# Optimization experiments

Measured on AMD Instinct MI355X. Metric: run time of the kernel, lower is better.

The kernel has to match this reference:

```python
import jax, jax.numpy as jnp
import numpy as np

DIM = 32
B, H, W = 4, 256, 256


def conv1x1(x, w, b):
    # x: [B,C,H,W], w: [O,C], b: [O]
    return jnp.einsum('bchw,oc->bohw', x, w) + b[None, :, None, None]


def conv3x3(x, w, b):
    # x: [B,C,H,W], w: [O,C,3,3]
    out = jax.lax.conv_general_dilated(
        x, w, window_strides=(1, 1), padding='SAME',
        dimension_numbers=('NCHW', 'OIHW', 'NCHW'))
    return out + b[None, :, None, None]


def fft2d(x):
    # fft2 over last two dims, then fftshift over ALL dims (torch default)
    f = jnp.fft.fftshift(jnp.fft.fft2(x, norm='ortho'))
    return jnp.concatenate([f.real, f.imag], axis=1)  # [B,2C,H,W]


def ifft2d(x):
    f = jnp.fft.ifftshift(x)  # over ALL dims (torch default)
    re, im = jnp.split(f, 2, axis=1)
    c = jax.lax.complex(re, im)
    return jnp.abs(jnp.fft.ifft2(c, norm='ortho'))  # [B,C,H,W]


def setup_inputs() -> dict:
    key = jax.random.key(0)
    ks = jax.random.split(key, 16)
    C = DIM
    s = 0.02  # small init keeps the global-HW dot products in a sane softmax range
    inp = {
        'x': jax.random.normal(ks[0], (B, C, H, W), jnp.float32),
        'y': jax.random.normal(ks[1], (B, C, H, W), jnp.float32),
        'wq': jax.random.normal(ks[2], (C, C), jnp.float32) * s,
        'bq': jnp.zeros((C,), jnp.float32),
        'wk': jax.random.normal(ks[3], (C, C), jnp.float32) * s,
        'bk': jnp.zeros((C,), jnp.float32),
        'wv': jax.random.normal(ks[4], (C, C), jnp.float32) * s,
        'bv': jnp.zeros((C,), jnp.float32),
        'wd': jax.random.normal(ks[5], (C, C), jnp.float32) * s,
        'bd': jnp.zeros((C,), jnp.float32),
        'wc': jax.random.normal(ks[6], (2 * C, 2 * C, 3, 3), jnp.float32) * s,
        'bc': jnp.zeros((2 * C,), jnp.float32),
        'wi': jax.random.normal(ks[7], (2 * C, 2 * C, 3, 3), jnp.float32) * s,
        'bi': jnp.zeros((2 * C,), jnp.float32),
    }
    return inp


def reference(x, y, wq, bq, wk, bk, wv, bv, wd, bd, wc, bc, wi, bi):
    b, c, h, w = x.shape
    xq = conv1x1(x, wq, bq).reshape(b, c, h * w)            # [B,C,HW]
    dft = conv3x3(fft2d(conv1x1(y, wd, bd)), wc, bc)        # [B,2C,H,W]
    yk, yv = jnp.split(dft, 2, axis=1)
    yk = conv1x1(yk, wk, bk).reshape(b, c, h * w)
    yv = conv1x1(yv, wv, bv).reshape(b, c, h * w)
    att = jnp.einsum('bcn,bdn->bcd', xq, yk)                # [B,C,C]
    att = jax.nn.softmax(att, axis=1)                       # softmax over dim=1 (as in torch)
    out = jnp.einsum('bcd,bdn->bcn', att, yv).reshape(b, c, h, w)
    out = out + ifft2d(conv3x3(jax.nn.relu(dft), wi, bi))
    return out
```

## Files before the change

### kernel.cpp

```cpp
#include <hip/hip_runtime.h>
#include <math.h>

#define HW_ (256*256)
#define CH 32
#define CH2 64
#define BATCH 4

typedef short bf16x8 __attribute__((ext_vector_type(8)));
typedef float f32x4 __attribute__((ext_vector_type(4)));

__device__ __forceinline__ unsigned short f2bf(float f) {
    union { float f; unsigned u; } v; v.f = f;
    unsigned r = v.u + 0x7fffu + ((v.u >> 16) & 1u);
    return (unsigned short)(r >> 16);
}
__device__ __forceinline__ float bf2f(unsigned h) {
    union { unsigned u; float f; } v; v.u = h << 16;
    return v.f;
}

__device__ __forceinline__ int ctof_slot(int s) {
    return s < 16 ? s + 16 : s < 32 ? s + 32 : s < 48 ? s - 32 : s - 16;
}

__device__ __forceinline__ float2 cmul(float2 a, float2 b) {
    return make_float2(a.x*b.x - a.y*b.y, a.x*b.y + a.y*b.x);
}

__device__ __forceinline__ void build_tw4(float2* tw, float sign) {
    int tid = threadIdx.x;
    float ang = sign * 6.2831853071795864769f * (float)tid / 256.0f;
    float s, c; sincosf(ang, &s, &c);
    tw[tid] = make_float2(c, s);
}

template<int SGN>
__device__ __forceinline__ void fft16_reg(float2* x, const float2* tw) {
    float2 u[16];
    #pragma unroll
    for (int m0 = 0; m0 < 4; ++m0) {
        float2 x0 = x[m0], x1 = x[m0+4], x2 = x[m0+8], x3 = x[m0+12];
        float2 t0 = make_float2(x0.x+x2.x, x0.y+x2.y);
        float2 t1 = make_float2(x0.x-x2.x, x0.y-x2.y);
        float2 t2 = make_float2(x1.x+x3.x, x1.y+x3.y);
        float2 t3 = make_float2(x1.x-x3.x, x1.y-x3.y);
        float2 r  = make_float2(-SGN*t3.y, SGN*t3.x);
        u[m0*4+0] = make_float2(t0.x+t2.x, t0.y+t2.y);
        u[m0*4+1] = make_float2(t1.x+r.x,  t1.y+r.y);
        u[m0*4+2] = make_float2(t0.x-t2.x, t0.y-t2.y);
        u[m0*4+3] = make_float2(t1.x-r.x,  t1.y-r.y);
    }
    #pragma unroll
    for (int m0 = 1; m0 < 4; ++m0)
        #pragma unroll
        for (int a = 1; a < 4; ++a)
            u[m0*4+a] = cmul(u[m0*4+a], tw[(16*m0*a) & 255]);
    #pragma unroll
    for (int a = 0; a < 4; ++a) {
        float2 x0 = u[a], x1 = u[4+a], x2 = u[8+a], x3 = u[12+a];
        float2 t0 = make_float2(x0.x+x2.x, x0.y+x2.y);
        float2 t1 = make_float2(x0.x-x2.x, x0.y-x2.y);
        float2 t2 = make_float2(x1.x+x3.x, x1.y+x3.y);
        float2 t3 = make_float2(x1.x-x3.x, x1.y-x3.y);
        float2 r  = make_float2(-SGN*t3.y, SGN*t3.x);
        x[a]    = make_float2(t0.x+t2.x, t0.y+t2.y);
        x[a+4]  = make_float2(t1.x+r.x,  t1.y+r.y);
        x[a+8]  = make_float2(t0.x-t2.x, t0.y-t2.y);
        x[a+12] = make_float2(t1.x-r.x,  t1.y-r.y);
    }
}

template<int SGN>
__device__ __forceinline__ void fft_core16(float2* A, const float2* tw) {
    const int tid = threadIdx.x;
    const int l = tid >> 4;
    const int d = tid & 15;
    const int base = l*257;
    float2 x[16];
    #pragma unroll
    for (int n1 = 0; n1 < 16; ++n1) x[n1] = A[base + n1*16 + d];
    fft16_reg<SGN>(x, tw);
    #pragma unroll
    for (int k0 = 1; k0 < 16; ++k0) x[k0] = cmul(x[k0], tw[d*k0]);
    #pragma unroll
    for (int k0 = 0; k0 < 16; ++k0) A[base + k0*16 + ((d + k0) & 15)] = x[k0];
    __syncthreads();
    #pragma unroll
    for (int n0 = 0; n0 < 16; ++n0) x[n0] = A[base + d*16 + ((n0 + d) & 15)];
    fft16_reg<SGN>(x, tw);
    #pragma unroll
    for (int k1 = 0; k1 < 16; ++k1) A[base + d + k1*16] = x[k1];
    __syncthreads();
}

__global__ __launch_bounds__(256) void k_fft_fwd1(const unsigned short* __restrict__ yd, ushort2* __restrict__ CAt) {
    __shared__ float2 A[16*257];
    __shared__ float2 tw[256];
    build_tw4(tw, -1.0f);
    int blk = blockIdx.x;
    int bc = blk >> 4, h0 = (blk & 15) << 4;
    const float sc = 1.0f/16.0f;
    const unsigned short* src = yd + (size_t)bc*HW_ + (size_t)h0*256;
    for (int idx = threadIdx.x; idx < 16*256; idx += 256) {
        int l = idx >> 8, w = idx & 255;
        A[l*257 + w] = make_float2(bf2f(src[l*256 + w])*sc, 0.0f);
    }
    __syncthreads();
    fft_core16<-1>(A, tw);
    int t = threadIdx.x;
    ushort2* dst = CAt + (size_t)bc*HW_ + (size_t)t*256 + h0;
    #pragma unroll
    for (int l = 0; l < 16; ++l) {
        float2 v = A[l*257 + t];
        dst[l] = make_ushort2(f2bf(v.x), f2bf(v.y));
    }
}

__global__ __launch_bounds__(256) void k_fft_fwd2(const ushort2* __restrict__ CAt, unsigned short* __restrict__ FSH) {
    __shared__ float2 A[16*257];
    __shared__ float2 tw[256];
    build_tw4(tw, -1.0f);
    int blk = blockIdx.x;
    int b = blk >> 9, chalf = (blk >> 8) & 1, w = blk & 255;
    const float sc = 1.0f/16.0f;
    const ushort2* src = CAt + (((size_t)(b*32 + chalf*16))*256 + w)*256;
    for (int idx = threadIdx.x; idx < 16*256; idx += 256) {
        int l = idx >> 8, h = idx & 255;
        ushort2 v = src[(size_t)l*HW_ + h];
        A[l*257 + h] = make_float2(bf2f(v.x)*sc, bf2f(v.y)*sc);
    }
    __syncthreads();
    fft_core16<-1>(A, tw);
    int t = threadIdx.x;
    int bt = (b + 2) & 3;
    int ht = (t + 128) & 255;
    int wt = (w + 128) & 255;
    unsigned short pk[32];
    #pragma unroll
    for (int l = 0; l < 16; ++l) {
        float2 v = A[l*257 + t];
        pk[l]      = f2bf(v.x);
        pk[16 + l] = f2bf(v.y);
    }
    unsigned short* dst = FSH + ((((size_t)bt*256 + ht)*256 + wt)*64 + chalf*32);
    uint4* d4 = (uint4*)dst;
    const uint4* s4 = (const uint4*)pk;
    d4[0] = s4[0]; d4[1] = s4[1]; d4[2] = s4[2]; d4[3] = s4[3];
}

__global__ __launch_bounds__(256) void k_wpack2(const float* __restrict__ wc, const float* __restrict__ wi,
                                                unsigned short* __restrict__ d1, unsigned short* __restrict__ d2) {
    int i = blockIdx.x*256 + threadIdx.x;
    int half = i >= 36864;
    int j = i - half*36864;
    int tap = j >> 12, rem = j & 4095, oc = rem >> 6, s = rem & 63;
    if (half) {
        d2[j] = f2bf(wi[((size_t)(oc*64 + s))*9 + tap]);
    } else {
        int ic = ctof_slot(s);
        d1[j] = f2bf(wc[((size_t)(oc*64 + ic))*9 + tap]);
    }
}

template<int MODE>
__global__ __launch_bounds__(256) void k_conv3(const unsigned short* __restrict__ in_cl,
                                               const unsigned short* __restrict__ wpk,
                                               const float* __restrict__ bias,
                                               unsigned short* __restrict__ outp) {
    __shared__ __align__(16) char Xs[3168*16];
    int tid = threadIdx.x;
    int blk = blockIdx.x;
    int wseg = blk & 3, hg = (blk >> 2) & 63, b = blk >> 8;
    int h0 = hg*4, w0 = wseg*64;

    for (int gl = tid; gl < 3168; gl += 256) {
        int slot = gl / 528;
        int rem  = gl - slot*528;
        int col  = rem >> 3, hseg = rem & 7;
        int hh = h0 - 1 + slot;
        int wcol = w0 - 1 + col;
        uint4 v = make_uint4(0,0,0,0);
        if (hh >= 0 && hh < 256 && wcol >= 0 && wcol < 256) {
            v = *(const uint4*)(in_cl + (((size_t)(b*256 + hh)*256 + wcol)*64) + hseg*8);
            if (MODE == 1) {
                unsigned* pv = (unsigned*)&v;
                #pragma unroll
                for (int q = 0; q < 4; ++q) {
                    unsigned a = pv[q];
                    unsigned lo = a & 0xffffu, hi = a >> 16;
                    if (lo & 0x8000u) lo = 0;
                    if (hi & 0x8000u) hi = 0;
                    pv[q] = lo | (hi << 16);
                }
            }
        }
        *(uint4*)(Xs + ((gl << 4) ^ ((col & 7) << 4))) = v;
    }
    __syncthreads();

    int lane = tid & 63;
    int wv = tid >> 6;
    int l16 = lane & 15, lq = lane >> 4;

    f32x4 acc[4][4];
    #pragma unroll
    for (int i = 0; i < 4; ++i)
        #pragma unroll
        for (int j = 0; j < 4; ++j) acc[i][j] = (f32x4)0.0f;

    #pragma unroll
    for (int dy = 0; dy < 3; ++dy) {
        int slot = wv + dy;
        #pragma unroll
        for (int dx = 0; dx < 3; ++dx) {
            int tap = dy*3 + dx;
            #pragma unroll
            for (int kk = 0; kk < 2; ++kk) {
                int hseg = kk*4 + lq;
                bf16x8 xf[4], wf[4];
                #pragma unroll
                for (int j = 0; j < 4; ++j) {
                    int col = j*16 + l16 + dx;
                    int g = slot*528 + col*8 + hseg;
                    xf[j] = *(const bf16x8*)(Xs + ((g << 4) ^ ((col & 7) << 4)));
                }
                #pragma unroll
                for (int i = 0; i < 4; ++i) {
                    int oc = i*16 + l16;
                    wf[i] = *(const bf16x8*)(wpk + (size_t)tap*4096 + oc*64 + hseg*8);
                    #pragma unroll
                    for (int j = 0; j < 4; ++j) {
                        if (MODE == 0)
                            acc[i][j] = __builtin_amdgcn_mfma_f32_16x16x32_bf16(wf[i], xf[j], acc[i][j], 0, 0, 0);
                        else
                            acc[i][j] = __builtin_amdgcn_mfma_f32_16x16x32_bf16(xf[j], wf[i], acc[i][j], 0, 0, 0);
                    }
                }
            }
        }
    }

    int h = h0 + wv;
    if (MODE == 0) {
        #pragma unroll
        for (int j = 0; j < 4; ++j) {
            int px = w0 + j*16 + l16;
            unsigned short* orow = outp + (((size_t)b*256 + h)*256 + px)*64;
            #pragma unroll
            for (int i = 0; i < 4; ++i) {
                int oc0 = i*16 + lq*4;
                float4 bv = *(const float4*)(bias + oc0);
                unsigned short c0 = f2bf(acc[i][j][0] + bv.x);
                unsigned short c1 = f2bf(acc[i][j][1] + bv.y);
                unsigned short c2 = f2bf(acc[i][j][2] + bv.z);
                unsigned short c3 = f2bf(acc[i][j][3] + bv.w);
                uint2 u;
                u.x = (unsigned)c0 | ((unsigned)c1 << 16);
                u.y = (unsigned)c2 | ((unsigned)c3 << 16);
                *(uint2*)(orow + oc0) = u;
            }
        }
    } else {
        #pragma unroll
        for (int i = 0; i < 4; ++i) {
            int oc = i*16 + l16;
            float bv = bias[oc];
            unsigned short* oplane = outp + ((size_t)b*64 + oc)*HW_ + (size_t)h*256;
            #pragma unroll
            for (int j = 0; j < 4; ++j) {
                int px0 = w0 + j*16 + lq*4;
                unsigned short c0 = f2bf(acc[i][j][0] + bv);
                unsigned short c1 = f2bf(acc[i][j][1] + bv);
                unsigned short c2 = f2bf(acc[i][j][2] + bv);
                unsigned short c3 = f2bf(acc[i][j][3] + bv);
                uint2 u;
                u.x = (unsigned)c0 | ((unsigned)c1 << 16);
                u.y = (unsigned)c2 | ((unsigned)c3 << 16);
                *(uint2*)(oplane + px0) = u;
            }
        }
    }
}

__global__ __launch_bounds__(256) void k_conv1x1(const float* __restrict__ in, const float* __restrict__ w,
                                                 const float* __restrict__ bias, unsigned short* __restrict__ out) {
    __shared__ float ts[32*257];
    int blk = blockIdx.x; int b = blk >> 8, h = blk & 255;
    int tid = threadIdx.x;
    const float* src = in + (size_t)b*CH*HW_ + (size_t)h*256;
    for (int idx = tid; idx < 32*256; idx += 256) {
        int c = idx >> 8, ww = idx & 255;
        ts[c*257 + ww] = src[(size_t)c*HW_ + ww];
    }
    __syncthreads();
    float acc[32];
    #pragma unroll
    for (int o = 0; o < 32; ++o) acc[o] = bias[o];
    for (int c = 0; c < 32; ++c) {
        float v = ts[c*257 + tid];
        #pragma unroll
        for (int o = 0; o < 32; ++o) acc[o] += w[o*32 + c] * v;
    }
    unsigned short* dst = out + (size_t)b*CH*HW_ + (size_t)h*256 + tid;
    #pragma unroll
    for (int o = 0; o < 32; ++o) dst[(size_t)o*HW_] = f2bf(acc[o]);
}

__global__ __launch_bounds__(256) void k_gram(const float* __restrict__ x, const unsigned short* __restrict__ dcl,
                                              float* __restrict__ Mpart, float* __restrict__ Sxp, float* __restrict__ Sdp) {
    __shared__ float mred[1024];
    __shared__ float sxred[32];
    __shared__ float sdred[32];
    int blk = blockIdx.x;
    int b = blk >> 7, chunk = blk & 127;
    int tid = threadIdx.x, lane = tid & 63, wv = tid >> 6;
    int l16 = lane & 15, lq = lane >> 4;
    for (int idx = tid; idx < 1024; idx += 256) mred[idx] = 0.0f;
    if (tid < 32) { sxred[tid] = 0.0f; sdred[tid] = 0.0f; }
    __syncthreads();

    const float* xb0 = x + (size_t)b*CH*HW_ + (size_t)l16*HW_;
    const float* xb1 = xb0 + (size_t)16*HW_;
    const unsigned short* db = dcl + (size_t)b*HW_*64;

    f32x4 acc[2][2];
    #pragma unroll
    for (int i = 0; i < 2; ++i)
        #pragma unroll
        for (int j = 0; j < 2; ++j) acc[i][j] = (f32x4)0.0f;
    float sx0 = 0, sx1 = 0, sd0 = 0, sd1 = 0;

    int pxw = chunk*512 + wv*128;
    #pragma unroll
    for (int ks = 0; ks < 4; ++ks) {
        int px = pxw + ks*32 + lq*8;
        float4 xa = *(const float4*)(xb0 + px);
        float4 xc = *(const float4*)(xb0 + px + 4);
        float4 ya = *(const float4*)(xb1 + px);
        float4 yc = *(const float4*)(xb1 + px + 4);
        bf16x8 a0, a1, b0, b1;
        const float* pxa = (const float*)&xa;
        const float* pxc = (const float*)&xc;
        const float* pya = (const float*)&ya;
        const float* pyc = (const float*)&yc;
        #pragma unroll
        for (int j = 0; j < 4; ++j) {
            a0[j]   = (short)f2bf(pxa[j]);  sx0 += pxa[j];
            a0[4+j] = (short)f2bf(pxc[j]);  sx0 += pxc[j];
            a1[j]   = (short)f2bf(pya[j]);  sx1 += pya[j];
            a1[4+j] = (short)f2bf(pyc[j]);  sx1 += pyc[j];
        }
        const unsigned short* dbp = db + (size_t)px*64 + l16;
        #pragma unroll
        for (int j = 0; j < 8; ++j) {
            unsigned short v0 = dbp[j*64];
            unsigned short v1 = dbp[j*64 + 16];
            b0[j] = (short)v0;  sd0 += bf2f(v0);
            b1[j] = (short)v1;  sd1 += bf2f(v1);
        }
        acc[0][0] = __builtin_amdgcn_mfma_f32_16x16x32_bf16(a0, b0, acc[0][0], 0, 0, 0);
        acc[0][1] = __builtin_amdgcn_mfma_f32_16x16x32_bf16(a0, b1, acc[0][1], 0, 0, 0);
        acc[1][0] = __builtin_amdgcn_mfma_f32_16x16x32_bf16(a1, b0, acc[1][0], 0, 0, 0);
        acc[1][1] = __builtin_amdgcn_mfma_f32_16x16x32_bf16(a1, b1, acc[1][1], 0, 0, 0);
    }

    #pragma unroll
    for (int fi = 0; fi < 2; ++fi)
        #pragma unroll
        for (int fj = 0; fj < 2; ++fj)
            #pragma unroll
            for (int r = 0; r < 4; ++r)
                atomicAdd(&mred[(fi*16 + lq*4 + r)*32 + fj*16 + l16], acc[fi][fj][r]);

    sx0 += __shfl_xor(sx0, 16); sx0 += __shfl_xor(sx0, 32);
    sx1 += __shfl_xor(sx1, 16); sx1 += __shfl_xor(sx1, 32);
    sd0 += __shfl_xor(sd0, 16); sd0 += __shfl_xor(sd0, 32);
    sd1 += __shfl_xor(sd1, 16); sd1 += __shfl_xor(sd1, 32);
    if (lane < 16) {
        atomicAdd(&sxred[l16], sx0);
        atomicAdd(&sxred[l16 + 16], sx1);
        atomicAdd(&sdred[l16], sd0);
        atomicAdd(&sdred[l16 + 16], sd1);
    }
    __syncthreads();

    float* mp = Mpart + ((size_t)(b*128 + chunk))*1024;
    for (int idx = tid; idx < 1024; idx += 256) mp[idx] = mred[idx];
    if (tid < 32) {
        Sxp[(b*128 + chunk)*32 + tid] = sxred[tid];
        Sdp[(b*128 + chunk)*32 + tid] = sdred[tid];
    }
}

__global__ __launch_bounds__(256) void k_att(const float* __restrict__ Mpart, const float* __restrict__ Sxp,
                                              const float* __restrict__ Sdp,
                                              const float* __restrict__ wq, const float* __restrict__ bq,
                                              const float* __restrict__ wk, const float* __restrict__ bk,
                                              const float* __restrict__ wv, const float* __restrict__ bv,
                                              float* __restrict__ att2, float* __restrict__ sout) {
    __shared__ float Mls[1024], T1[1024], attls[32*33];
    __shared__ float wqs[1024], wks[1024], wvs[1024];
    __shared__ float q1[32], k1[32], sxs[32], sds[32];
    int tid = threadIdx.x;
    int b = blockIdx.x;
    for (int idx = tid; idx < 1024; idx += 256) { wqs[idx] = wq[idx]; wks[idx] = wk[idx]; wvs[idx] = wv[idx]; }
    #pragma unroll
    for (int q = 0; q < 4; ++q) {
        int o = tid + q*256;
        float s = 0;
        for (int c = 0; c < 128; ++c) s += Mpart[((size_t)(b*128 + c))*1024 + o];
        Mls[o] = s;
    }
    if (tid < 32) { float s = 0; for (int c = 0; c < 128; ++c) s += Sxp[(b*128 + c)*32 + tid]; sxs[tid] = s; }
    else if (tid < 64) { int e = tid - 32; float s = 0; for (int c = 0; c < 128; ++c) s += Sdp[(b*128 + c)*32 + e]; sds[e] = s; }
    __syncthreads();
    if (tid < 32) { float s=0; for (int a=0;a<32;++a) s += wqs[tid*32+a]*sxs[a]; q1[tid]=s; }
    else if (tid < 64) { int d=tid-32; float s=0; for (int e=0;e<32;++e) s += wks[d*32+e]*sds[e]; k1[d]=s; }
    for (int idx = tid; idx < 1024; idx += 256) {
        int c = idx >> 5, e = idx & 31;
        float s = 0;
        for (int a=0;a<32;++a) s += wqs[c*32+a]*Mls[a*32+e];
        T1[idx] = s;
    }
    __syncthreads();
    for (int idx = tid; idx < 1024; idx += 256) {
        int c = idx >> 5, d = idx & 31;
        float s = 0;
        for (int e=0;e<32;++e) s += T1[c*32+e]*wks[d*32+e];
        s += bq[c]*k1[d] + bk[d]*q1[c] + 65536.0f*bq[c]*bk[d];
        attls[c*33+d] = s;
    }
    __syncthreads();
    if (tid < 32) {
        int d = tid;
        float mx = -1e30f;
        for (int c=0;c<32;++c) mx = fmaxf(mx, attls[c*33+d]);
        float sum = 0;
        for (int c=0;c<32;++c) { float e_ = expf(attls[c*33+d]-mx); attls[c*33+d]=e_; sum+=e_; }
        float inv = 1.0f/sum;
        for (int c=0;c<32;++c) attls[c*33+d] *= inv;
    }
    __syncthreads();
    for (int idx = tid; idx < 1024; idx += 256) {
        int c = idx >> 5, e = idx & 31;
        float s = 0;
        for (int d=0; d<32; ++d) s += attls[c*33+d]*wvs[d*32+e];
        att2[b*1024 + idx] = s;
    }
    if (tid < 32) {
        float s=0; for (int d=0;d<32;++d) s += attls[tid*33+d]*bv[d];
        sout[b*32+tid] = s;
    }
}

__global__ __launch_bounds__(256) void k_fft_inv1(const unsigned short* __restrict__ G, ushort2* __restrict__ Z1T) {
    __shared__ float2 A[16*257];
    __shared__ float2 tw[256];
    build_tw4(tw, 1.0f);
    int blk = blockIdx.x;
    int bc = blk >> 4, w0 = (blk & 15) << 4;
    int b = bc >> 5, c = bc & 31;
    int bs = (b + 2) & 3;
    const float sc = 1.0f/16.0f;
    const unsigned short* gre = G + ((size_t)(bs*CH2 + c + 32))*HW_;
    const unsigned short* gim = G + ((size_t)(bs*CH2 + c))*HW_;
    for (int idx = threadIdx.x; idx < 16*256; idx += 256) {
        int h = idx >> 4, l = idx & 15;
        int hs = (h + 128) & 255;
        int ws = (w0 + l + 128) & 255;
        A[l*257 + h] = make_float2(bf2f(gre[(size_t)hs*256 + ws])*sc, bf2f(gim[(size_t)hs*256 + ws])*sc);
    }
    __syncthreads();
    fft_core16<1>(A, tw);
    ushort2* dst = Z1T + (size_t)bc*HW_;
    for (int idx = threadIdx.x; idx < 16*256; idx += 256) {
        int l = idx >> 8, h = idx & 255;
        float2 v = A[l*257 + h];
        dst[(size_t)(w0 + l)*256 + h] = make_ushort2(f2bf(v.x), f2bf(v.y));
    }
}

__global__ __launch_bounds__(256) void k_fft_inv2(const ushort2* __restrict__ Z1T, unsigned short* __restrict__ Mag) {
    __shared__ float2 A[16*257];
    __shared__ float2 tw[256];
    build_tw4(tw, 1.0f);
    int blk = blockIdx.x;
    int bc = blk >> 4, h0 = (blk & 15) << 4;
    const float sc = 1.0f/16.0f;
    const ushort2* src = Z1T + (size_t)bc*HW_ + h0;
    for (int idx = threadIdx.x; idx < 16*256; idx += 256) {
        int w = idx >> 4, l = idx & 15;
        ushort2 v = src[(size_t)w*256 + l];
        A[l*257 + w] = make_float2(bf2f(v.x)*sc, bf2f(v.y)*sc);
    }
    __syncthreads();
    fft_core16<1>(A, tw);
    unsigned short* dst = Mag + (size_t)bc*HW_ + (size_t)h0*256;
    for (int idx = threadIdx.x; idx < 16*256; idx += 256) {
        int l = idx >> 8, w = idx & 255;
        float2 v = A[l*257 + w];
        dst[l*256 + w] = f2bf(sqrtf(v.x*v.x + v.y*v.y));
    }
}

__global__ __launch_bounds__(256) void k_out(const unsigned short* __restrict__ dcl, const float* __restrict__ att2,
                                             const float* __restrict__ sv, const unsigned short* __restrict__ Mag,
                                             float* __restrict__ out) {
    __shared__ __align__(16) float A2ls[1024];
    __shared__ float svls[32];
    int blk = blockIdx.x; int b = blk >> 8, h = blk & 255;
    int tid = threadIdx.x;
    for (int idx = tid; idx < 1024; idx += 256) A2ls[idx] = att2[b*1024 + idx];
    if (tid < 32) svls[tid] = sv[b*32 + tid];
    __syncthreads();
    int px = tid;
    const uint4* dvp = (const uint4*)(dcl + ((((size_t)b*256 + h)*256 + px)*64 + 32));
    uint4 d0 = dvp[0], d1 = dvp[1];
    unsigned u[8] = {d0.x, d0.y, d0.z, d0.w, d1.x, d1.y, d1.z, d1.w};
    float dv[32];
    #pragma unroll
    for (int i = 0; i < 8; ++i) {
        dv[2*i]   = bf2f(u[i] & 0xffffu);
        dv[2*i+1] = bf2f(u[i] >> 16);
    }
    float accv[32];
    #pragma unroll
    for (int c = 0; c < 32; ++c) accv[c] = svls[c];
    #pragma unroll
    for (int q = 0; q < 8; ++q) {
        #pragma unroll
        for (int c = 0; c < 32; ++c) {
            float4 a4 = *(const float4*)&A2ls[c*32 + q*4];
            accv[c] += a4.x*dv[q*4] + a4.y*dv[q*4+1] + a4.z*dv[q*4+2] + a4.w*dv[q*4+3];
        }
    }
    const unsigned short* mb = Mag + (size_t)b*CH*HW_ + (size_t)h*256 + px;
    float* ob = out + (size_t)b*CH*HW_ + (size_t)h*256 + px;
    #pragma unroll
    for (int c = 0; c < 32; ++c) ob[(size_t)c*HW_] = accv[c] + bf2f(mb[(size_t)c*HW_]);
}

extern "C" void kernel_launch(void* const* d_in, const int* in_sizes, int n_in,
                              void* d_out, int out_size, void* d_ws, size_t ws_size,
                              hipStream_t stream) {
    const float* x  = (const float*)d_in[0];
    const float* y  = (const float*)d_in[1];
    const float* wq = (const float*)d_in[2];
    const float* bq = (const float*)d_in[3];
    const float* wk = (const float*)d_in[4];
    const float* bk = (const float*)d_in[5];
    const float* wv = (const float*)d_in[6];
    const float* bv = (const float*)d_in[7];
    const float* wd = (const float*)d_in[8];
    const float* bd = (const float*)d_in[9];
    const float* wc = (const float*)d_in[10];
    const float* bc = (const float*)d_in[11];
    const float* wi = (const float*)d_in[12];
    const float* bi = (const float*)d_in[13];
    float* out = (float*)d_out;

    char* ws = (char*)d_ws;
    size_t o = 0;
    unsigned short* R1   = (unsigned short*)(ws + o); o += (size_t)BATCH*CH*HW_*2;
    ushort2*        CAt  = (ushort2*)(ws + o);        o += (size_t)BATCH*CH*HW_*4;
    unsigned short* FSHc = (unsigned short*)(ws + o); o += (size_t)BATCH*CH2*HW_*2;
    unsigned short* DFTc = (unsigned short*)(ws + o); o += (size_t)BATCH*CH2*HW_*2;
    unsigned short* Gpl  = (unsigned short*)(ws + o); o += (size_t)BATCH*CH2*HW_*2;
    unsigned short* wpk1 = (unsigned short*)(ws + o); o += 9*64*64*2;
    unsigned short* wpk2 = (unsigned short*)(ws + o); o += 9*64*64*2;
    float*          Mpart= (float*)(ws + o);          o += (size_t)512*1024*4;
    float*          Sxp  = (float*)(ws + o);          o += 512*32*4;
    float*          Sdp  = (float*)(ws + o);          o += 512*32*4;
    float*          A2b  = (float*)(ws + o);          o += 4096*4;
    float*          Svb  = (float*)(ws + o);          o += 128*4;
    if (ws_size < o) return;

    ushort2*        Z1T = CAt;
    unsigned short* Mag = R1;

    k_wpack2<<<288, 256, 0, stream>>>(wc, wi, wpk1, wpk2);
    k_conv1x1<<<1024, 256, 0, stream>>>(y, wd, bd, R1);
    k_fft_fwd1<<<2048, 256, 0, stream>>>(R1, CAt);
    k_fft_fwd2<<<2048, 256, 0, stream>>>(CAt, FSHc);
    k_conv3<0><<<1024, 256, 0, stream>>>(FSHc, wpk1, bc, DFTc);
    k_conv3<1><<<1024, 256, 0, stream>>>(DFTc, wpk2, bi, Gpl);
    k_gram<<<512, 256, 0, stream>>>(x, DFTc, Mpart, Sxp, Sdp);
    k_att<<<4, 256, 0, stream>>>(Mpart, Sxp, Sdp, wq, bq, wk, bk, wv, bv, A2b, Svb);
    k_fft_inv1<<<2048, 256, 0, stream>>>(Gpl, Z1T);
    k_fft_inv2<<<2048, 256, 0, stream>>>(Z1T, Mag);
    k_out<<<1024, 256, 0, stream>>>(DFTc, A2b, Svb, Mag, out);
}
```

Measured before the change: 319.5 us.

## Stage conv3x3 weights in LDS and prefetch input rows per dy step

The 3x3 conv kernel now keeps one dy-row of weights (3 taps) in shared memory and only 4 of the 6 input rows in a ring buffer. It register-prefetches the next input row and weight slice from global memory while the MFMAs for the current dy run. This replaces per-MFMA global weight loads with swizzled LDS reads and shrinks LDS use, but adds two barriers per dy step. The forward FFT pass 1 also switches to vectorized uint2 loads and packed uint4 stores.

```diff
diff --git a/kernel.cpp b/kernel.cpp
--- a/kernel.cpp
+++ b/kernel.cpp
@@ -25,6 +25,19 @@
 
 __device__ __forceinline__ float2 cmul(float2 a, float2 b) {
     return make_float2(a.x*b.x - a.y*b.y, a.x*b.y + a.y*b.x);
+}
+
+__device__ __forceinline__ uint4 relu_bf16x8(uint4 v) {
+    unsigned* pv = (unsigned*)&v;
+    #pragma unroll
+    for (int q = 0; q < 4; ++q) {
+        unsigned a = pv[q];
+        unsigned lo = a & 0xffffu, hi = a >> 16;
+        if (lo & 0x8000u) lo = 0;
+        if (hi & 0x8000u) hi = 0;
+        pv[q] = lo | (hi << 16);
+    }
+    return v;
 }
 
 __device__ __forceinline__ void build_tw4(float2* tw, float sign) {
@@ -101,19 +114,27 @@
     int bc = blk >> 4, h0 = (blk & 15) << 4;
     const float sc = 1.0f/16.0f;
     const unsigned short* src = yd + (size_t)bc*HW_ + (size_t)h0*256;
-    for (int idx = threadIdx.x; idx < 16*256; idx += 256) {
-        int l = idx >> 8, w = idx & 255;
-        A[l*257 + w] = make_float2(bf2f(src[l*256 + w])*sc, 0.0f);
+    for (int idx = threadIdx.x; idx < 16*64; idx += 256) {
+        int l = idx >> 6, w4 = (idx & 63) << 2;
+        uint2 v = *(const uint2*)(src + l*256 + w4);
+        A[l*257 + w4+0] = make_float2(bf2f(v.x & 0xffffu)*sc, 0.0f);
+        A[l*257 + w4+1] = make_float2(bf2f(v.x >> 16)*sc, 0.0f);
+        A[l*257 + w4+2] = make_float2(bf2f(v.y & 0xffffu)*sc, 0.0f);
+        A[l*257 + w4+3] = make_float2(bf2f(v.y >> 16)*sc, 0.0f);
     }
     __syncthreads();
     fft_core16<-1>(A, tw);
     int t = threadIdx.x;
-    ushort2* dst = CAt + (size_t)bc*HW_ + (size_t)t*256 + h0;
+    unsigned short pk[32];
     #pragma unroll
     for (int l = 0; l < 16; ++l) {
         float2 v = A[l*257 + t];
-        dst[l] = make_ushort2(f2bf(v.x), f2bf(v.y));
-    }
+        pk[2*l]   = f2bf(v.x);
+        pk[2*l+1] = f2bf(v.y);
+    }
+    uint4* d4 = (uint4*)(CAt + (size_t)bc*HW_ + (size_t)t*256 + h0);
+    const uint4* s4 = (const uint4*)pk;
+    d4[0] = s4[0]; d4[1] = s4[1]; d4[2] = s4[2]; d4[3] = s4[3];
 }
 
 __global__ __launch_bounds__(256) void k_fft_fwd2(const ushort2* __restrict__ CAt, unsigned short* __restrict__ FSH) {
@@ -167,13 +188,16 @@
                                                const unsigned short* __restrict__ wpk,
                                                const float* __restrict__ bias,
                                                unsigned short* __restrict__ outp) {
-    __shared__ __align__(16) char Xs[3168*16];
+    __shared__ __align__(16) char Xs[2112*16];
+    __shared__ __align__(16) char Ws[1536*16];
     int tid = threadIdx.x;
     int blk = blockIdx.x;
     int wseg = blk & 3, hg = (blk >> 2) & 63, b = blk >> 8;
     int h0 = hg*4, w0 = wseg*64;
 
-    for (int gl = tid; gl < 3168; gl += 256) {
+    const uint4* wsrc = (const uint4*)wpk;
+
+    for (int gl = tid; gl < 2112; gl += 256) {
         int slot = gl / 528;
         int rem  = gl - slot*528;
         int col  = rem >> 3, hseg = rem & 7;
@@ -182,19 +206,15 @@
         uint4 v = make_uint4(0,0,0,0);
         if (hh >= 0 && hh < 256 && wcol >= 0 && wcol < 256) {
             v = *(const uint4*)(in_cl + (((size_t)(b*256 + hh)*256 + wcol)*64) + hseg*8);
-            if (MODE == 1) {
-                unsigned* pv = (unsigned*)&v;
-                #pragma unroll
-                for (int q = 0; q < 4; ++q) {
-                    unsigned a = pv[q];
-                    unsigned lo = a & 0xffffu, hi = a >> 16;
-                    if (lo & 0x8000u) lo = 0;
-                    if (hi & 0x8000u) hi = 0;
-                    pv[q] = lo | (hi << 16);
-                }
-            }
+            if (MODE == 1) v = relu_bf16x8(v);
         }
         *(uint4*)(Xs + ((gl << 4) ^ ((col & 7) << 4))) = v;
+    }
+    #pragma unroll
+    for (int q = 0; q < 6; ++q) {
+        int gw = tid + q*256;
+        int oc = (gw >> 3) & 63;
+        *(uint4*)(Ws + ((gw << 4) ^ ((oc & 7) << 4))) = wsrc[gw];
     }
     __syncthreads();
 
@@ -208,12 +228,41 @@
         #pragma unroll
         for (int j = 0; j < 4; ++j) acc[i][j] = (f32x4)0.0f;
 
-    #pragma unroll
     for (int dy = 0; dy < 3; ++dy) {
-        int slot = wv + dy;
+        uint4 xr0 = make_uint4(0,0,0,0), xr1 = make_uint4(0,0,0,0), xr2 = make_uint4(0,0,0,0);
+        uint4 wr[6];
+        if (dy < 2) {
+            int hh = h0 + dy + 2;
+            bool hv = hh < 256;
+            {
+                int gl = tid;
+                int col = gl >> 3, hseg = gl & 7;
+                int wcol = w0 - 1 + col;
+                if (hv && wcol >= 0 && wcol < 256)
+                    xr0 = *(const uint4*)(in_cl + (((size_t)(b*256 + hh)*256 + wcol)*64) + hseg*8);
+            }
+            {
+                int gl = tid + 256;
+                int col = gl >> 3, hseg = gl & 7;
+                int wcol = w0 - 1 + col;
+                if (hv && wcol >= 0 && wcol < 256)
+                    xr1 = *(const uint4*)(in_cl + (((size_t)(b*256 + hh)*256 + wcol)*64) + hseg*8);
+            }
+            if (tid < 16) {
+                int gl = tid + 512;
+                int col = gl >> 3, hseg = gl & 7;
+                int wcol = w0 - 1 + col;
+                if (hv && wcol < 256)
+                    xr2 = *(const uint4*)(in_cl + (((size_t)(b*256 + hh)*256 + wcol)*64) + hseg*8);
+            }
+            #pragma unroll
+            for (int q = 0; q < 6; ++q)
+                wr[q] = wsrc[(dy+1)*1536 + tid + q*256];
+        }
+
+        int slot = (wv + dy) & 3;
         #pragma unroll
         for (int dx = 0; dx < 3; ++dx) {
-            int tap = dy*3 + dx;
             #pragma unroll
             for (int kk = 0; kk < 2; ++kk) {
                 int hseg = kk*4 + lq;
@@ -227,7 +276,8 @@
                 #pragma unroll
                 for (int i = 0; i < 4; ++i) {
                     int oc = i*16 + l16;
-                    wf[i] = *(const bf16x8*)(wpk + (size_t)tap*4096 + oc*64 + hseg*8);
+                    int lw = dx*512 + oc*8 + hseg;
+                    wf[i] = *(const bf16x8*)(Ws + ((lw << 4) ^ ((oc & 7) << 4)));
                     #pragma unroll
                     for (int j = 0; j < 4; ++j) {
                         if (MODE == 0)
@@ -237,6 +287,39 @@
                     }
                 }
             }
+        }
+
+        if (dy < 2) {
+            __syncthreads();
+            int slotn = (dy + 3) & 3;
+            {
+                int gl = tid;
+                int col = gl >> 3;
+                uint4 v = (MODE == 1) ? relu_bf16x8(xr0) : xr0;
+                int g = slotn*528 + gl;
+                *(uint4*)(Xs + ((g << 4) ^ ((col & 7) << 4))) = v;
+            }
+            {
+                int gl = tid + 256;
+                int col = gl >> 3;
+                uint4 v = (MODE == 1) ? relu_bf16x8(xr1) : xr1;
+                int g = slotn*528 + gl;
+                *(uint4*)(Xs + ((g << 4) ^ ((col & 7) << 4))) = v;
+            }
+            if (tid < 16) {
+                int gl = tid + 512;
+                int col = gl >> 3;
+                uint4 v = (MODE == 1) ? relu_bf16x8(xr2) : xr2;
+                int g = slotn*528 + gl;
+                *(uint4*)(Xs + ((g << 4) ^ ((col & 7) << 4))) = v;
+            }
+            #pragma unroll
+            for (int q = 0; q < 6; ++q) {
+                int gw = tid + q*256;
+                int oc = (gw >> 3) & 63;
+                *(uint4*)(Ws + ((gw << 4) ^ ((oc & 7) << 4))) = wr[q];
+            }
+            __syncthreads();
         }
     }
 
```

Measured after the change: 278.3 us. 12.9% less time.
